# Kernel tuning notes

Measured on AMD Instinct MI355X. Metric: run time of the kernel, lower is better.

## Reference

```python
import jax, jax.numpy as jnp
import numpy as np

N_HEAD = 32
N_KV_HEAD = 8
ROPE_THETA = 500000.0


def rotate_half(x):
    d = x.shape[-1] // 2
    return jnp.concatenate((-x[..., d:], x[..., :d]), axis=-1)


def setup_inputs() -> dict:
    key = jax.random.key(0)
    ks = jax.random.split(key, 5)
    C = 2048
    B, T = 2, 2048
    s = 1.0 / np.sqrt(C)
    return {
        "x": jax.random.normal(ks[0], (B, T, C), dtype=jnp.float32),
        "Wq": jax.random.normal(ks[1], (C, C), dtype=jnp.float32) * s,
        "Wk": jax.random.normal(ks[2], (C, 512), dtype=jnp.float32) * s,
        "Wv": jax.random.normal(ks[3], (C, 512), dtype=jnp.float32) * s,
        "Wo": jax.random.normal(ks[4], (C, C), dtype=jnp.float32) * s,
    }


def reference(x, Wq, Wk, Wv, Wo):
    B, T, C = x.shape
    H, KV = N_HEAD, N_KV_HEAD
    D = C // H
    n_rep = H // KV

    q = (x @ Wq).reshape(B, T, H, D).transpose(0, 2, 1, 3)   # [B,H,T,D]
    k = (x @ Wk).reshape(B, T, KV, D).transpose(0, 2, 1, 3)  # [B,KV,T,D]
    v = (x @ Wv).reshape(B, T, KV, D).transpose(0, 2, 1, 3)  # [B,KV,T,D]

    # RoPE: cos/sin of shape [1,1,T,D], broadcast over batch and heads
    inv_freq = 1.0 / (ROPE_THETA ** (jnp.arange(0, D, 2, dtype=jnp.float32) / D))
    freqs = jnp.arange(T, dtype=jnp.float32)[:, None] * inv_freq[None, :]  # [T,D/2]
    emb = jnp.concatenate((freqs, freqs), axis=-1)  # [T,D]
    cos = jnp.cos(emb)[None, None].astype(x.dtype)
    sin = jnp.sin(emb)[None, None].astype(x.dtype)

    q = q * cos + rotate_half(q) * sin
    k = k * cos + rotate_half(k) * sin

    # repeat_kv (GQA expansion): [B,KV,T,D] -> [B,H,T,D]
    k = jnp.repeat(k, n_rep, axis=1)
    v = jnp.repeat(v, n_rep, axis=1)

    scale = 1.0 / jnp.sqrt(jnp.asarray(D, dtype=x.dtype))
    scores = jnp.einsum("bhqd,bhkd->bhqk", q, k) * scale  # [B,H,T,T]
    causal = jnp.tril(jnp.ones((T, T), dtype=bool))
    scores = jnp.where(causal[None, None], scores, jnp.finfo(scores.dtype).min)
    attn = jax.nn.softmax(scores, axis=-1)
    y = jnp.einsum("bhqk,bhkd->bhqd", attn, v)  # [B,H,T,D]
    y = y.transpose(0, 2, 1, 3).reshape(B, T, C)
    return y @ Wo
```

## Files before the change

### kernel.cpp

```cpp
#include <hip/hip_runtime.h>

using u16 = unsigned short;
using u32 = unsigned int;

typedef __attribute__((ext_vector_type(8))) __bf16 bf16x8;
typedef __attribute__((ext_vector_type(4))) float f32x4;
typedef __attribute__((ext_vector_type(16))) float f32x16;

#define DEVI __device__ __forceinline__

DEVI float bf2f(u16 u) {
  union { u32 i; float f; } v; v.i = ((u32)u) << 16; return v.f;
}
DEVI u16 f2bf(float f) {
  union { float f; u32 u; } v; v.f = f;
  u32 u = v.u;
  u32 r = (u + 0x7fffu + ((u >> 16) & 1u)) >> 16;
  return (u16)r;
}
DEVI u32 pkbf(float a, float b) {
  union { __bf16 h[2]; u32 u; } t;
  t.h[0] = (__bf16)a; t.h[1] = (__bf16)b;
  return t.u;
}

DEVI void gload16(const u16* g, u16* l) {
  __builtin_amdgcn_global_load_lds(
      (const __attribute__((address_space(1))) void*)g,
      (__attribute__((address_space(3))) void*)l, 16, 0, 0);
}

__global__ __launch_bounds__(256) void cvt_bf16_f32(const float* __restrict__ in,
                                                    u16* __restrict__ out, int n8) {
  int i = blockIdx.x * 256 + threadIdx.x;
  if (i >= n8) return;
  const float4* fin = (const float4*)in;
  float4 a = fin[i * 2], b = fin[i * 2 + 1];
  u16 o[8] = {f2bf(a.x), f2bf(a.y), f2bf(a.z), f2bf(a.w),
              f2bf(b.x), f2bf(b.y), f2bf(b.z), f2bf(b.w)};
  ((uint4*)out)[i] = *(const uint4*)o;
}

__global__ __launch_bounds__(256) void transpose_cvt64(const float* __restrict__ in,
                                                       u16* __restrict__ out,
                                                       int R, int Cc) {
  __shared__ u16 tile[64][72];
  int c0 = blockIdx.x * 64, r0 = blockIdx.y * 64;
  int t = threadIdx.x;
  {
    int row = t >> 2, part = t & 3;
    const float* src = in + (size_t)(r0 + row) * Cc + c0 + part * 16;
    float4 f0 = ((const float4*)src)[0];
    float4 f1 = ((const float4*)src)[1];
    float4 f2 = ((const float4*)src)[2];
    float4 f3 = ((const float4*)src)[3];
    u16 v[16] = {f2bf(f0.x), f2bf(f0.y), f2bf(f0.z), f2bf(f0.w),
                 f2bf(f1.x), f2bf(f1.y), f2bf(f1.z), f2bf(f1.w),
                 f2bf(f2.x), f2bf(f2.y), f2bf(f2.z), f2bf(f2.w),
                 f2bf(f3.x), f2bf(f3.y), f2bf(f3.z), f2bf(f3.w)};
    *(uint4*)&tile[row][part * 16]     = ((const uint4*)v)[0];
    *(uint4*)&tile[row][part * 16 + 8] = ((const uint4*)v)[1];
  }
  __syncthreads();
  {
    int c = t & 63, rq = t >> 6;
    u16 v[16];
#pragma unroll
    for (int i = 0; i < 16; i++) v[i] = tile[rq * 16 + i][c];
    u16* dst = out + (size_t)(c0 + c) * R + r0 + rq * 16;
    ((uint4*)dst)[0] = ((const uint4*)v)[0];
    ((uint4*)dst)[1] = ((const uint4*)v)[1];
  }
}

__global__ __launch_bounds__(256) void transpose_sl64(const u16* __restrict__ in, int ldin,
                                                      u16* __restrict__ out,
                                                      int R, int Cc) {
  __shared__ u16 tile[64][72];
  int c0 = blockIdx.x * 64, r0 = blockIdx.y * 64;
  int t = threadIdx.x;
  {
    int row = t >> 2, part = t & 3;
    const u16* src = in + (size_t)(r0 + row) * ldin + c0 + part * 16;
    uint4 a = ((const uint4*)src)[0];
    uint4 b = ((const uint4*)src)[1];
    *(uint4*)&tile[row][part * 16]     = a;
    *(uint4*)&tile[row][part * 16 + 8] = b;
  }
  __syncthreads();
  {
    int c = t & 63, rq = t >> 6;
    u16 v[16];
#pragma unroll
    for (int i = 0; i < 16; i++) v[i] = tile[rq * 16 + i][c];
    u16* dst = out + (size_t)(c0 + c) * R + r0 + rq * 16;
    ((uint4*)dst)[0] = ((const uint4*)v)[0];
    ((uint4*)dst)[1] = ((const uint4*)v)[1];
  }
}

__global__ __launch_bounds__(256) void rope_v(u16* __restrict__ X, int ld, int h4shift,
                                              float scale, int total) {
  int idx = blockIdx.x * 256 + threadIdx.x;
  if (idx >= total) return;
  int hq   = idx & ((1 << h4shift) - 1);
  int row  = idx >> h4shift;
  int head = hq >> 2;
  int d0   = (hq & 3) * 8;
  int tpos = row & 2047;
  size_t base = (size_t)row * ld + head * 64 + d0;
  uint4 lo = *(const uint4*)(X + base);
  uint4 hi = *(const uint4*)(X + base + 32);
  const u16* lp = (const u16*)&lo;
  const u16* hp = (const u16*)&hi;
  float ang = (float)tpos * exp2f(-(float)d0 * 0.59161152f);
  u16 o0[8], o1[8];
#pragma unroll
  for (int i = 0; i < 8; i++) {
    float s, c;
    __sincosf(ang, &s, &c);
    s *= scale; c *= scale;
    float x0 = bf2f(lp[i]);
    float x1 = bf2f(hp[i]);
    o0[i] = f2bf(x0 * c - x1 * s);
    o1[i] = f2bf(x1 * c + x0 * s);
    ang *= 0.6636011f;
  }
  *(uint4*)(X + base)      = *(const uint4*)o0;
  *(uint4*)(X + base + 32) = *(const uint4*)o1;
}

DEVI void cstore(u16* C, size_t idx, float v)   { C[idx] = f2bf(v); }
DEVI void cstore(float* C, size_t idx, float v) { C[idx] = v; }

template <typename TO>
__global__ __launch_bounds__(256) void gemm128(const u16* __restrict__ A,
                                               const u16* __restrict__ Bt,
                                               TO* __restrict__ C,
                                               int M, int N, int K) {
  __shared__ u16 As[2 * 128 * 32];
  __shared__ u16 Bs[2 * 128 * 32];
  int tid = threadIdx.x, wid = tid >> 6, lane = tid & 63;
  int quad = lane >> 4, l15 = lane & 15;
  int m0 = blockIdx.y * 128, n0 = blockIdx.x * 128;
  int wm = (wid >> 1) * 64, wn = (wid & 1) * 64;

  int r0s = wid * 16 + (lane >> 2);
  int r1s = 64 + wid * 16 + (lane >> 2);
  int cblk = lane & 3;
  int cs0 = (cblk ^ ((r0s >> 1) & 3)) * 8;
  int cs1 = (cblk ^ ((r1s >> 1) & 3)) * 8;
  u16* lA0 = As + wid * 512 + lane * 8;
  u16* lA1 = As + (4 + wid) * 512 + lane * 8;
  u16* lB0 = Bs + wid * 512 + lane * 8;
  u16* lB1 = Bs + (4 + wid) * 512 + lane * 8;
  const u16* gA0 = A + (size_t)(m0 + r0s) * K + cs0;
  const u16* gA1 = A + (size_t)(m0 + r1s) * K + cs1;
  const u16* gB0 = Bt + (size_t)(n0 + r0s) * K + cs0;
  const u16* gB1 = Bt + (size_t)(n0 + r1s) * K + cs1;

  f32x4 acc[4][4];
  for (int i = 0; i < 4; i++)
    for (int j = 0; j < 4; j++) acc[i][j] = f32x4{0.f, 0.f, 0.f, 0.f};

  gload16(gA0, lA0);
  gload16(gA1, lA1);
  gload16(gB0, lB0);
  gload16(gB1, lB1);
  __builtin_amdgcn_s_waitcnt(0x0F70);
  __syncthreads();

  int cur = 0;
  for (int k0 = 0; k0 < K; k0 += 32) {
    int nb = cur ^ 1;
    if (k0 + 32 < K) {
      gload16(gA0 + k0 + 32, lA0 + nb * 4096);
      gload16(gA1 + k0 + 32, lA1 + nb * 4096);
      gload16(gB0 + k0 + 32, lB0 + nb * 4096);
      gload16(gB1 + k0 + 32, lB1 + nb * 4096);
    }
    const u16* Ab = As + cur * 4096;
    const u16* Bb = Bs + cur * 4096;
    bf16x8 af[4], bf_[4];
    for (int mi = 0; mi < 4; mi++) {
      int row = wm + mi * 16 + l15;
      af[mi] = *(const bf16x8*)(Ab + row * 32 + ((quad ^ ((row >> 1) & 3)) * 8));
    }
    for (int ni = 0; ni < 4; ni++) {
      int row = wn + ni * 16 + l15;
      bf_[ni] = *(const bf16x8*)(Bb + row * 32 + ((quad ^ ((row >> 1) & 3)) * 8));
    }
    for (int mi = 0; mi < 4; mi++)
      for (int ni = 0; ni < 4; ni++)
        acc[mi][ni] = __builtin_amdgcn_mfma_f32_16x16x32_bf16(af[mi], bf_[ni], acc[mi][ni], 0, 0, 0);
    __builtin_amdgcn_s_waitcnt(0x0F70);
    __syncthreads();
    cur = nb;
  }
  for (int mi = 0; mi < 4; mi++)
    for (int ni = 0; ni < 4; ni++)
      for (int r = 0; r < 4; r++) {
        int row = m0 + wm + mi * 16 + quad * 4 + r;
        int col = n0 + wn + ni * 16 + l15;
        cstore(C, (size_t)row * N + col, acc[mi][ni][r]);
      }
}

__global__ __launch_bounds__(256) void attn64(const u16* __restrict__ QKV,
                                              const u16* __restrict__ Vt,
                                              u16* __restrict__ Y) {
  __shared__ u16 Ks[2 * 64 * 64];
  __shared__ u16 Vst[2 * 64 * 64];

  int tid = threadIdx.x, wid = tid >> 6, lane = tid & 63;
  int l31 = lane & 31, hi = lane >> 5;
  int bh = blockIdx.y, b = bh >> 5, h = bh & 31, kvh = h >> 2;
  int p = blockIdx.x;

  int kr  = wid * 8 + (lane >> 3);
  int kgn = lane & 7;
  const u16* gK0 = QKV + (size_t)(b * 2048 + kr) * 3072 + 2048 + kvh * 64
                 + ((kgn ^ (kr & 7)) * 8);
  u16* lK0 = Ks + wid * 512 + lane * 8;

  int vr = tid >> 3, vg = tid & 7;
  const u16* gV0 = Vt + (size_t)(kvh * 64 + vr) * 4096 + b * 2048 + vg * 8;
  u16* lV0 = Vst + vr * 64 + ((vg ^ (vr & 7)) * 8);

  for (int pass = 0; pass < 2; pass++) {
    int j   = pass ? (15 - p) : p;
    int q0w = j * 128 + wid * 32;
    int qg  = q0w + l31;

    bf16x8 qf[4];
    {
      const u16* qp = QKV + (size_t)(b * 2048 + qg) * 3072 + h * 64 + hi * 8;
#pragma unroll
      for (int dh = 0; dh < 4; dh++) qf[dh] = *(const bf16x8*)(qp + dh * 16);
    }

    f32x16 o0, o1;
#pragma unroll
    for (int i = 0; i < 16; i++) { o0[i] = 0.f; o1[i] = 0.f; }
    float zsum = 0.f;

    int nkt = 2 * (j + 1);

    {
      uint4 va = *(const uint4*)(gV0);
      uint4 vb = *(const uint4*)(gV0 + 32 * 4096);
      gload16(gK0, lK0);
      gload16(gK0 + 32 * 3072, lK0 + 2048);
      __builtin_amdgcn_s_waitcnt(0x0F70);
      *(uint4*)(lV0)        = va;
      *(uint4*)(lV0 + 2048) = vb;
    }
    __syncthreads();

    int cur = 0;
    for (int kt = 0; kt < nkt; kt++) {
      int kbase = kt * 64;
      int nxt = cur ^ 1;
      bool more = (kt + 1 < nkt);
      uint4 va, vb;
      if (more) {
        size_t ko = (size_t)(kbase + 64);
        va = *(const uint4*)(gV0 + ko);
        vb = *(const uint4*)(gV0 + 32 * 4096 + ko);
        gload16(gK0 + ko * 3072, lK0 + nxt * 4096);
        gload16(gK0 + ko * 3072 + 32 * 3072, lK0 + nxt * 4096 + 2048);
      }

      const u16* Kb = Ks + cur * 4096;
      const u16* Vb = Vst + cur * 4096;
#pragma unroll
      for (int sub = 0; sub < 2; sub++) {
        int kb = kbase + sub * 32;
        if (kb > q0w) break;

        f32x16 s;
#pragma unroll
        for (int i = 0; i < 16; i++) s[i] = 0.f;
#pragma unroll
        for (int dh = 0; dh < 4; dh++) {
          int g = (dh * 2 + hi) ^ (l31 & 7);
          bf16x8 kf = *(const bf16x8*)(Kb + (sub * 32 + l31) * 64 + g * 8);
          s = __builtin_amdgcn_mfma_f32_32x32x16_bf16(kf, qf[dh], s, 0, 0, 0);
        }

        float pb[16];
        if (kb < q0w) {
#pragma unroll
          for (int r = 0; r < 16; r++) {
            float pv = exp2f(s[r]);
            zsum += pv;
            pb[r] = pv;
          }
        } else {
#pragma unroll
          for (int r = 0; r < 16; r++) {
            int key = kb + (r & 3) + 8 * (r >> 2) + 4 * hi;
            float pv = (key <= qg) ? exp2f(s[r]) : 0.f;
            zsum += pv;
            pb[r] = pv;
          }
        }

#pragma unroll
        for (int kk = 0; kk < 2; kk++) {
          const float* pp = pb + kk * 8;
          u32 a01 = pkbf(pp[0], pp[1]);
          u32 a23 = pkbf(pp[2], pp[3]);
          u32 a45 = pkbf(pp[4], pp[5]);
          u32 a67 = pkbf(pp[6], pp[7]);
          asm volatile("v_permlane32_swap_b32 %0, %1" : "+v"(a01), "+v"(a45));
          asm volatile("v_permlane32_swap_b32 %0, %1" : "+v"(a23), "+v"(a67));
          union { u32 w[4]; bf16x8 v; } pf;
          pf.w[0] = a01; pf.w[1] = a23; pf.w[2] = a45; pf.w[3] = a67;
          int kgr = sub * 4 + kk * 2 + hi;
          const u16* vp = Vb + l31 * 64 + ((kgr ^ (l31 & 7)) * 8);
          bf16x8 v0 = *(const bf16x8*)(vp);
          bf16x8 v1 = *(const bf16x8*)(vp + 2048);
          o0 = __builtin_amdgcn_mfma_f32_32x32x16_bf16(pf.v, v0, o0, 0, 0, 0);
          o1 = __builtin_amdgcn_mfma_f32_32x32x16_bf16(pf.v, v1, o1, 0, 0, 0);
        }
      }

      if (more) {
        __builtin_amdgcn_s_waitcnt(0x0F70);
        *(uint4*)(lV0 + nxt * 4096)        = va;
        *(uint4*)(lV0 + nxt * 4096 + 2048) = vb;
      }
      __syncthreads();
      cur = nxt;
    }

    float zf = zsum + __shfl_xor(zsum, 32);

#pragma unroll
    for (int r = 0; r < 16; r++) {
      int qr = (r & 3) + 8 * (r >> 2) + 4 * hi;
      float zr = __shfl(zf, qr, 64);
      float inv = 1.f / zr;
      size_t row = (size_t)(b * 2048 + q0w + qr);
      Y[row * 2048 + h * 64 + l31]      = f2bf(o0[r] * inv);
      Y[row * 2048 + h * 64 + 32 + l31] = f2bf(o1[r] * inv);
    }
  }
}

extern "C" void kernel_launch(void* const* d_in, const int* in_sizes, int n_in,
                              void* d_out, int out_size, void* d_ws, size_t ws_size,
                              hipStream_t stream) {
  const float* x  = (const float*)d_in[0];
  const float* Wq = (const float*)d_in[1];
  const float* Wk = (const float*)d_in[2];
  const float* Wv = (const float*)d_in[3];
  const float* Wo = (const float*)d_in[4];
  float* outp = (float*)d_out;

  u16* xb    = (u16*)d_ws;
  u16* WqkvT = xb + 8388608;
  u16* QKV   = WqkvT + 6291456;
  u16* Vt    = QKV + 12582912;
  u16* Yb    = xb;
  u16* WoT   = WqkvT;

  cvt_bf16_f32<<<4096, 256, 0, stream>>>(x, xb, 1048576);

  transpose_cvt64<<<dim3(32, 32), 256, 0, stream>>>(Wq, WqkvT, 2048, 2048);
  transpose_cvt64<<<dim3(8, 32), 256, 0, stream>>>(Wk, WqkvT + (size_t)2048 * 2048, 2048, 512);
  transpose_cvt64<<<dim3(8, 32), 256, 0, stream>>>(Wv, WqkvT + (size_t)2560 * 2048, 2048, 512);

  gemm128<u16><<<dim3(24, 32), 256, 0, stream>>>(xb, WqkvT, QKV, 4096, 3072, 2048);

  rope_v<<<2048, 256, 0, stream>>>(QKV, 3072, 7, 0.18033688f, 4096 * 128);
  rope_v<<<512, 256, 0, stream>>>(QKV + 2048, 3072, 5, 1.0f, 4096 * 32);

  transpose_sl64<<<dim3(8, 64), 256, 0, stream>>>(QKV + 2560, 3072, Vt, 4096, 512);

  attn64<<<dim3(8, 64), 256, 0, stream>>>(QKV, Vt, Yb);

  transpose_cvt64<<<dim3(32, 32), 256, 0, stream>>>(Wo, WoT, 2048, 2048);
  gemm128<float><<<dim3(16, 32), 256, 0, stream>>>(Yb, WoT, outp, 4096, 2048, 2048);
}
```

Before: 329.6 us.

## Merge weight-transpose and RoPE launches; compute softmax denominator via MFMA

The three Wq/Wk/Wv transpose-convert launches become one kernel that picks its source by block index, and the two RoPE launches become one. In attention, the per-lane scalar sum of probabilities followed by cross-lane shuffles is replaced by an extra MFMA of the bf16 P tile against a ones vector. The score MFMA chain also starts from a zero constant. This cuts launch overhead and scalar adds/shuffles, at the cost of one more MFMA per PV step and a denominator summed from bf16-rounded probabilities.

```diff
diff --git a/kernel.cpp b/kernel.cpp
--- a/kernel.cpp
+++ b/kernel.cpp
@@ -41,12 +41,8 @@
   ((uint4*)out)[i] = *(const uint4*)o;
 }
 
-__global__ __launch_bounds__(256) void transpose_cvt64(const float* __restrict__ in,
-                                                       u16* __restrict__ out,
-                                                       int R, int Cc) {
-  __shared__ u16 tile[64][72];
-  int c0 = blockIdx.x * 64, r0 = blockIdx.y * 64;
-  int t = threadIdx.x;
+DEVI void tcvt64_body(const float* in, u16* out, int R, int Cc, int c0, int r0, int t,
+                      u16 (*tile)[72]) {
   {
     int row = t >> 2, part = t & 3;
     const float* src = in + (size_t)(r0 + row) * Cc + c0 + part * 16;
@@ -73,6 +69,28 @@
   }
 }
 
+__global__ __launch_bounds__(256) void transpose_cvt64(const float* __restrict__ in,
+                                                       u16* __restrict__ out,
+                                                       int R, int Cc) {
+  __shared__ u16 tile[64][72];
+  tcvt64_body(in, out, R, Cc, blockIdx.x * 64, blockIdx.y * 64, threadIdx.x, tile);
+}
+
+__global__ __launch_bounds__(256) void transpose_wqkv(const float* __restrict__ Wq,
+                                                      const float* __restrict__ Wk,
+                                                      const float* __restrict__ Wv,
+                                                      u16* __restrict__ out) {
+  __shared__ u16 tile[64][72];
+  int bx = blockIdx.x;
+  const float* in;
+  u16* dst;
+  int Cc, c0;
+  if (bx < 32)      { in = Wq; dst = out;                        Cc = 2048; c0 = bx * 64; }
+  else if (bx < 40) { in = Wk; dst = out + (size_t)2048 * 2048;  Cc = 512;  c0 = (bx - 32) * 64; }
+  else              { in = Wv; dst = out + (size_t)2560 * 2048;  Cc = 512;  c0 = (bx - 40) * 64; }
+  tcvt64_body(in, dst, 2048, Cc, c0, blockIdx.y * 64, threadIdx.x, tile);
+}
+
 __global__ __launch_bounds__(256) void transpose_sl64(const u16* __restrict__ in, int ldin,
                                                       u16* __restrict__ out,
                                                       int R, int Cc) {
@@ -99,16 +117,13 @@
   }
 }
 
-__global__ __launch_bounds__(256) void rope_v(u16* __restrict__ X, int ld, int h4shift,
-                                              float scale, int total) {
-  int idx = blockIdx.x * 256 + threadIdx.x;
-  if (idx >= total) return;
+DEVI void rope_body(u16* X, int h4shift, float scale, int idx) {
   int hq   = idx & ((1 << h4shift) - 1);
   int row  = idx >> h4shift;
   int head = hq >> 2;
   int d0   = (hq & 3) * 8;
   int tpos = row & 2047;
-  size_t base = (size_t)row * ld + head * 64 + d0;
+  size_t base = (size_t)row * 3072 + head * 64 + d0;
   uint4 lo = *(const uint4*)(X + base);
   uint4 hi = *(const uint4*)(X + base + 32);
   const u16* lp = (const u16*)&lo;
@@ -128,6 +143,13 @@
   }
   *(uint4*)(X + base)      = *(const uint4*)o0;
   *(uint4*)(X + base + 32) = *(const uint4*)o1;
+}
+
+__global__ __launch_bounds__(256) void rope_fused(u16* __restrict__ QKV) {
+  const int NQ = 4096 * 128;
+  int idx = blockIdx.x * 256 + threadIdx.x;
+  if (idx < NQ) rope_body(QKV, 7, 0.18033688f, idx);
+  else          rope_body(QKV + 2048, 5, 1.0f, idx - NQ);
 }
 
 DEVI void cstore(u16* C, size_t idx, float v)   { C[idx] = f2bf(v); }
@@ -227,6 +249,17 @@
   const u16* gV0 = Vt + (size_t)(kvh * 64 + vr) * 4096 + b * 2048 + vg * 8;
   u16* lV0 = Vst + vr * 64 + ((vg ^ (vr & 7)) * 8);
 
+  f32x16 fzero;
+#pragma unroll
+  for (int i = 0; i < 16; i++) fzero[i] = 0.f;
+  bf16x8 onesf;
+  {
+    union { u16 w[8]; bf16x8 v; } t;
+#pragma unroll
+    for (int i = 0; i < 8; i++) t.w[i] = 0x3F80;
+    onesf = t.v;
+  }
+
   for (int pass = 0; pass < 2; pass++) {
     int j   = pass ? (15 - p) : p;
     int q0w = j * 128 + wid * 32;
@@ -239,10 +272,9 @@
       for (int dh = 0; dh < 4; dh++) qf[dh] = *(const bf16x8*)(qp + dh * 16);
     }
 
-    f32x16 o0, o1;
-#pragma unroll
-    for (int i = 0; i < 16; i++) { o0[i] = 0.f; o1[i] = 0.f; }
-    float zsum = 0.f;
+    f32x16 o0, o1, zacc;
+#pragma unroll
+    for (int i = 0; i < 16; i++) { o0[i] = 0.f; o1[i] = 0.f; zacc[i] = 0.f; }
 
     int nkt = 2 * (j + 1);
 
@@ -278,11 +310,10 @@
         int kb = kbase + sub * 32;
         if (kb > q0w) break;
 
-        f32x16 s;
-#pragma unroll
-        for (int i = 0; i < 16; i++) s[i] = 0.f;
-#pragma unroll
-        for (int dh = 0; dh < 4; dh++) {
+        bf16x8 kf0 = *(const bf16x8*)(Kb + (sub * 32 + l31) * 64 + (((0 * 2 + hi) ^ (l31 & 7)) * 8));
+        f32x16 s = __builtin_amdgcn_mfma_f32_32x32x16_bf16(kf0, qf[0], fzero, 0, 0, 0);
+#pragma unroll
+        for (int dh = 1; dh < 4; dh++) {
           int g = (dh * 2 + hi) ^ (l31 & 7);
           bf16x8 kf = *(const bf16x8*)(Kb + (sub * 32 + l31) * 64 + g * 8);
           s = __builtin_amdgcn_mfma_f32_32x32x16_bf16(kf, qf[dh], s, 0, 0, 0);
@@ -291,18 +322,12 @@
         float pb[16];
         if (kb < q0w) {
 #pragma unroll
-          for (int r = 0; r < 16; r++) {
-            float pv = exp2f(s[r]);
-            zsum += pv;
-            pb[r] = pv;
-          }
+          for (int r = 0; r < 16; r++) pb[r] = exp2f(s[r]);
         } else {
 #pragma unroll
           for (int r = 0; r < 16; r++) {
             int key = kb + (r & 3) + 8 * (r >> 2) + 4 * hi;
-            float pv = (key <= qg) ? exp2f(s[r]) : 0.f;
-            zsum += pv;
-            pb[r] = pv;
+            pb[r] = (key <= qg) ? exp2f(s[r]) : 0.f;
           }
         }
 
@@ -321,6 +346,7 @@
           const u16* vp = Vb + l31 * 64 + ((kgr ^ (l31 & 7)) * 8);
           bf16x8 v0 = *(const bf16x8*)(vp);
           bf16x8 v1 = *(const bf16x8*)(vp + 2048);
+          zacc = __builtin_amdgcn_mfma_f32_32x32x16_bf16(pf.v, onesf, zacc, 0, 0, 0);
           o0 = __builtin_amdgcn_mfma_f32_32x32x16_bf16(pf.v, v0, o0, 0, 0, 0);
           o1 = __builtin_amdgcn_mfma_f32_32x32x16_bf16(pf.v, v1, o1, 0, 0, 0);
         }
@@ -335,13 +361,10 @@
       cur = nxt;
     }
 
-    float zf = zsum + __shfl_xor(zsum, 32);
-
 #pragma unroll
     for (int r = 0; r < 16; r++) {
       int qr = (r & 3) + 8 * (r >> 2) + 4 * hi;
-      float zr = __shfl(zf, qr, 64);
-      float inv = 1.f / zr;
+      float inv = 1.f / zacc[r];
       size_t row = (size_t)(b * 2048 + q0w + qr);
       Y[row * 2048 + h * 64 + l31]      = f2bf(o0[r] * inv);
       Y[row * 2048 + h * 64 + 32 + l31] = f2bf(o1[r] * inv);
@@ -368,14 +391,11 @@
 
   cvt_bf16_f32<<<4096, 256, 0, stream>>>(x, xb, 1048576);
 
-  transpose_cvt64<<<dim3(32, 32), 256, 0, stream>>>(Wq, WqkvT, 2048, 2048);
-  transpose_cvt64<<<dim3(8, 32), 256, 0, stream>>>(Wk, WqkvT + (size_t)2048 * 2048, 2048, 512);
-  transpose_cvt64<<<dim3(8, 32), 256, 0, stream>>>(Wv, WqkvT + (size_t)2560 * 2048, 2048, 512);
+  transpose_wqkv<<<dim3(48, 32), 256, 0, stream>>>(Wq, Wk, Wv, WqkvT);
 
   gemm128<u16><<<dim3(24, 32), 256, 0, stream>>>(xb, WqkvT, QKV, 4096, 3072, 2048);
 
-  rope_v<<<2048, 256, 0, stream>>>(QKV, 3072, 7, 0.18033688f, 4096 * 128);
-  rope_v<<<512, 256, 0, stream>>>(QKV + 2048, 3072, 5, 1.0f, 4096 * 32);
+  rope_fused<<<2560, 256, 0, stream>>>(QKV);
 
   transpose_sl64<<<dim3(8, 64), 256, 0, stream>>>(QKV + 2560, 3072, Vt, 4096, 512);
 
```

Result: faster. 322.5 us (-2.1%).
